# Kernel tuning notes

Measured on AMD Instinct MI355X. Metric: run time of the kernel, lower is better.

## Reference

```python
import jax, jax.numpy as jnp
import numpy as np

B, S, H = 2, 2048, 2048
NUM_HEADS, HEAD_DIM, GROUP_SIZE = 16, 128, 4
NUM_KV_HEADS = NUM_HEADS // GROUP_SIZE
ROPE_THETA = 10000.0


def setup_inputs() -> dict:
    key = jax.random.key(0)
    ks = jax.random.split(key, 10)
    xavier = lambda k, fi, fo: jax.random.uniform(k, (fi, fo), jnp.float32,
                                                  -jnp.sqrt(6.0 / (fi + fo)), jnp.sqrt(6.0 / (fi + fo)))
    hidden_states = jax.random.normal(ks[0], (B, S, H), jnp.float32)
    # causal mask: 1.0 where attention is disallowed (strictly upper triangle)
    mask = jnp.triu(jnp.ones((S, S), jnp.float32), k=1)[None, None, :, :]
    mask = jnp.broadcast_to(mask, (B, 1, S, S))
    return {
        "hidden_states": hidden_states,
        "mask": mask,
        "Wq": xavier(ks[1], H, NUM_HEADS * HEAD_DIM), "bq": jnp.zeros((NUM_HEADS * HEAD_DIM,), jnp.float32),
        "Wk": xavier(ks[2], H, NUM_KV_HEADS * HEAD_DIM), "bk": jnp.zeros((NUM_KV_HEADS * HEAD_DIM,), jnp.float32),
        "Wv": xavier(ks[3], H, NUM_KV_HEADS * HEAD_DIM), "bv": jnp.zeros((NUM_KV_HEADS * HEAD_DIM,), jnp.float32),
        "Wo": xavier(ks[4], NUM_HEADS * HEAD_DIM, H), "bo": jnp.zeros((H,), jnp.float32),
    }


def _apply_rope(q, k):
    # q: [b, s, hq, d], k: [b, s, hk, d]
    s, d = q.shape[1], q.shape[-1]
    inv_freq = 1.0 / (ROPE_THETA ** (jnp.arange(0, d, 2, dtype=jnp.float32) / d))  # [d/2]
    angles = jnp.arange(s, dtype=jnp.float32)[:, None] * inv_freq[None, :]          # [s, d/2]
    cos = jnp.cos(angles)[None, :, None, :]  # [1, s, 1, d/2]
    sin = jnp.sin(angles)[None, :, None, :]

    def rot(x):
        x1, x2 = jnp.split(x, 2, axis=-1)
        return jnp.concatenate([x1 * cos - x2 * sin, x1 * sin + x2 * cos], axis=-1)

    return rot(q), rot(k)


def reference(hidden_states, mask, Wq, bq, Wk, bk, Wv, bv, Wo, bo):
    b, s, _ = hidden_states.shape
    scale = 1.0 / jnp.sqrt(jnp.float32(HEAD_DIM))

    q = (hidden_states @ Wq + bq).reshape(b, s, NUM_HEADS, HEAD_DIM)
    k = (hidden_states @ Wk + bk).reshape(b, s, NUM_KV_HEADS, HEAD_DIM)
    v = (hidden_states @ Wv + bv).reshape(b, s, NUM_KV_HEADS, HEAD_DIM)

    q, k = _apply_rope(q, k)

    q = jnp.transpose(q, (0, 2, 1, 3))  # [b, hq, s, d]
    k = jnp.transpose(k, (0, 2, 1, 3))  # [b, hk, s, d]
    v = jnp.transpose(v, (0, 2, 1, 3))

    new_past_key, new_past_value = k, v

    # GQA: repeat each KV head group_size times
    k_rep = jnp.repeat(k, GROUP_SIZE, axis=1)  # [b, hq, s, d]
    v_rep = jnp.repeat(v, GROUP_SIZE, axis=1)

    attn_scores = jnp.einsum('bhqd,bhkd->bhqk', q, k_rep) * scale  # [b, hq, s, s]
    attn_scores = attn_scores + mask * -1e9
    attn_probs = jax.nn.softmax(attn_scores, axis=-1)
    attn_output = jnp.einsum('bhqk,bhkd->bhqd', attn_probs, v_rep)

    attn_output = attn_output.transpose(0, 2, 1, 3).reshape(b, s, NUM_HEADS * HEAD_DIM)
    attn_output = attn_output @ Wo + bo
    return attn_output, new_past_key, new_past_value
```

## Files before the change

kernel.cpp:

```cpp
#include <hip/hip_runtime.h>
#include <stdint.h>

#define S_LEN 2048
#define HDIM  2048
#define N_HEADS 16
#define HEAD_D 128
#define N_KV 4

typedef unsigned short u16;
typedef __attribute__((ext_vector_type(8))) short bf16x8;
typedef __attribute__((ext_vector_type(4))) float f32x4;

__device__ __forceinline__ u16 f2bf(float f) {
  unsigned u = __float_as_uint(f);
  u += 0x7FFFu + ((u >> 16) & 1u);
  return (u16)(u >> 16);
}

__device__ __forceinline__ void gll16(void* lds, const void* gp) {
  __builtin_amdgcn_global_load_lds(
      (const __attribute__((address_space(1))) void*)gp,
      (__attribute__((address_space(3))) void*)lds, 16, 0, 0);
}

__global__ __launch_bounds__(256) void k_convert(const float* __restrict__ src,
                                                 u16* __restrict__ dst, int n4) {
  int i = blockIdx.x * 256 + threadIdx.x;
  if (i < n4) {
    float4 v = ((const float4*)src)[i];
    ushort4 o;
    o.x = f2bf(v.x); o.y = f2bf(v.y); o.z = f2bf(v.z); o.w = f2bf(v.w);
    ((ushort4*)dst)[i] = o;
  }
}

__global__ __launch_bounds__(256) void k_transpose_w(const float* __restrict__ W,
                                                     u16* __restrict__ Wt,
                                                     int K, int N) {
  __shared__ float tile[64][65];
  int k0 = blockIdx.x * 64, n0 = blockIdx.y * 64;
  int tr = threadIdx.x >> 6, tc = threadIdx.x & 63;
#pragma unroll
  for (int i = 0; i < 16; ++i) {
    int r = tr + i * 4;
    tile[r][tc] = W[(size_t)(k0 + r) * N + n0 + tc];
  }
  __syncthreads();
#pragma unroll
  for (int i = 0; i < 16; ++i) {
    int r = tr + i * 4;
    Wt[(size_t)(n0 + r) * K + k0 + tc] = f2bf(tile[tc][r]);
  }
}

__device__ __forceinline__ void gemm_tile_128(
    const u16* __restrict__ A, const u16* __restrict__ Bt,
    const float* __restrict__ bias, float* __restrict__ C,
    int m0, int n0, int K, int ldc) {
  __shared__ __align__(16) u16 sA[128 * 32];
  __shared__ __align__(16) u16 sB[128 * 32];
  const int tid = threadIdx.x;
  const int lane = tid & 63;
  const int wave = tid >> 6;
  const int quad = lane >> 4;
  const int l15 = lane & 15;
  const int wm = (wave >> 1) << 6;
  const int wn = (wave & 1) << 6;

  f32x4 acc[4][4];
#pragma unroll
  for (int i = 0; i < 4; ++i)
#pragma unroll
    for (int j = 0; j < 4; ++j)
      acc[i][j] = (f32x4){0.f, 0.f, 0.f, 0.f};

  for (int kk = 0; kk < K; kk += 32) {
    __syncthreads();
#pragma unroll
    for (int it = 0; it < 2; ++it) {
      int c = tid + (it << 8);
      int row = c >> 2;
      int ko = (c & 3) << 3;
      gll16((char*)sA + c * 16, A + (size_t)(m0 + row) * K + kk + ko);
      gll16((char*)sB + c * 16, Bt + (size_t)(n0 + row) * K + kk + ko);
    }
    __syncthreads();
    bf16x8 af[4], bfr[4];
#pragma unroll
    for (int i = 0; i < 4; ++i)
      af[i] = *(const bf16x8*)&sA[(wm + (i << 4) + l15) * 32 + quad * 8];
#pragma unroll
    for (int j = 0; j < 4; ++j)
      bfr[j] = *(const bf16x8*)&sB[(wn + (j << 4) + l15) * 32 + quad * 8];
#pragma unroll
    for (int i = 0; i < 4; ++i)
#pragma unroll
      for (int j = 0; j < 4; ++j)
        acc[i][j] = __builtin_amdgcn_mfma_f32_16x16x32_bf16(af[i], bfr[j], acc[i][j], 0, 0, 0);
  }

#pragma unroll
  for (int i = 0; i < 4; ++i) {
    int row = m0 + wm + (i << 4) + quad * 4;
#pragma unroll
    for (int j = 0; j < 4; ++j) {
      int col = n0 + wn + (j << 4) + l15;
      float bv = bias[col];
      float* cp = C + (size_t)row * ldc + col;
#pragma unroll
      for (int r = 0; r < 4; ++r)
        cp[(size_t)r * ldc] = acc[i][j][r] + bv;
    }
  }
}

__global__ __launch_bounds__(256) void k_gemm_qkv(
    const u16* __restrict__ X, const u16* __restrict__ Wqt,
    const u16* __restrict__ Wkt, const u16* __restrict__ Wvt,
    const float* __restrict__ bq, const float* __restrict__ bk,
    const float* __restrict__ bv, float* __restrict__ Qf,
    float* __restrict__ Kf, float* __restrict__ Vf) {
  int m0 = blockIdx.x << 7;
  int by = blockIdx.y;
  const u16* Bt; const float* bias; float* C; int n0, ldc;
  if (by < 16)      { Bt = Wqt; bias = bq; C = Qf; n0 = by << 7;        ldc = 2048; }
  else if (by < 20) { Bt = Wkt; bias = bk; C = Kf; n0 = (by - 16) << 7; ldc = 512;  }
  else              { Bt = Wvt; bias = bv; C = Vf; n0 = (by - 20) << 7; ldc = 512;  }
  gemm_tile_128(X, Bt, bias, C, m0, n0, 2048, ldc);
}

__global__ __launch_bounds__(256) void k_gemm_o(
    const u16* __restrict__ A, const u16* __restrict__ Wot,
    const float* __restrict__ bo, float* __restrict__ C) {
  gemm_tile_128(A, Wot, bo, C, blockIdx.x << 7, blockIdx.y << 7, 2048, 2048);
}

__global__ __launch_bounds__(256) void k_rope(
    const float* __restrict__ Qf, const float* __restrict__ Kf,
    u16* __restrict__ Qbf, u16* __restrict__ Kbf, float* __restrict__ outK) {
  const int bx = blockIdx.x;
  const int b = bx >> 11;
  const int s = bx & 2047;
  const int tid = threadIdx.x;
  const float qscale = 0.08838834764831845f;
  const float c1 = -13.287712379549449f / 64.f;

#pragma unroll
  for (int it = 0; it < 4; ++it) {
    int p = tid + (it << 8);
    int hh = p >> 6;
    int ii = p & 63;
    float ang = (float)s * exp2f((float)ii * c1);
    float cs, sn;
    sincosf(ang, &sn, &cs);
    const float* src = Qf + (size_t)bx * 2048 + hh * 128 + ii;
    float x1 = src[0], x2 = src[64];
    float o1 = (x1 * cs - x2 * sn) * qscale;
    float o2 = (x1 * sn + x2 * cs) * qscale;
    u16* dst = Qbf + ((size_t)(b * N_HEADS + hh) * S_LEN + s) * HEAD_D + ii;
    dst[0] = f2bf(o1);
    dst[64] = f2bf(o2);
  }
  {
    int hh = tid >> 6;
    int ii = tid & 63;
    float ang = (float)s * exp2f((float)ii * c1);
    float cs, sn;
    sincosf(ang, &sn, &cs);
    const float* src = Kf + (size_t)bx * 512 + hh * 128 + ii;
    float x1 = src[0], x2 = src[64];
    float o1 = x1 * cs - x2 * sn;
    float o2 = x1 * sn + x2 * cs;
    size_t idx = ((size_t)(b * N_KV + hh) * S_LEN + s) * HEAD_D + ii;
    Kbf[idx] = f2bf(o1);
    Kbf[idx + 64] = f2bf(o2);
    outK[idx] = o1;
    outK[idx + 64] = o2;
  }
}

__global__ __launch_bounds__(256) void k_vtrans(const float* __restrict__ Vf,
                                                u16* __restrict__ Vt,
                                                float* __restrict__ outV) {
  __shared__ float tile[64][65];
  int s0 = blockIdx.x * 64, d0 = blockIdx.y * 64;
  int z = blockIdx.z;
  int b = z >> 2, kvh = z & 3;
  int tr = threadIdx.x >> 6, tc = threadIdx.x & 63;
#pragma unroll
  for (int i = 0; i < 16; ++i) {
    int r = tr + i * 4;
    float v = Vf[(size_t)(b * S_LEN + s0 + r) * 512 + kvh * 128 + d0 + tc];
    tile[r][tc] = v;
    outV[((size_t)z * S_LEN + s0 + r) * HEAD_D + d0 + tc] = v;
  }
  __syncthreads();
#pragma unroll
  for (int i = 0; i < 16; ++i) {
    int r = tr + i * 4;
    Vt[((size_t)z * HEAD_D + d0 + r) * S_LEN + s0 + tc] = f2bf(tile[tc][r]);
  }
}

__global__ __launch_bounds__(256, 2) void k_attn(
    const u16* __restrict__ Qbf, const u16* __restrict__ Kbf,
    const u16* __restrict__ Vt, u16* __restrict__ attn) {
  __shared__ __align__(16) u16 smem[27136];
  u16* sK = smem;
  u16* sV = smem + 8704;
  u16* sP = smem + 17920;

  const int tid = threadIdx.x;
  const int lane = tid & 63;
  const int wave = tid >> 6;
  const int quad = lane >> 4;
  const int l15 = lane & 15;

  const int qt = blockIdx.x;
  const int b = blockIdx.y >> 4;
  const int h = blockIdx.y & 15;
  const int kvh = h >> 2;
  const int q0 = qt << 7;

  const u16* Qb = Qbf + ((size_t)(b * N_HEADS + h) * S_LEN + q0) * HEAD_D;
  const u16* Kb = Kbf + (size_t)(b * N_KV + kvh) * S_LEN * HEAD_D;
  const u16* Vb = Vt + (size_t)(b * N_KV + kvh) * HEAD_D * S_LEN;

  for (int it = 0; it < 9; ++it) {
    int c = tid + (it << 8);
    if (c < 2176) {
      int row = c / 17;
      int k16 = c - row * 17;
      gll16((char*)smem + c * 16, Qb + (size_t)row * HEAD_D + k16 * 8);
    }
  }
  __syncthreads();

  bf16x8 aq[2][4];
#pragma unroll
  for (int i = 0; i < 2; ++i)
#pragma unroll
    for (int kc = 0; kc < 4; ++kc)
      aq[i][kc] = *(const bf16x8*)&smem[(wave * 32 + i * 16 + l15) * 136 + kc * 32 + quad * 8];

  float mst[2][4], lst[2][4];
  f32x4 oacc[2][8];
#pragma unroll
  for (int i = 0; i < 2; ++i) {
#pragma unroll
    for (int r = 0; r < 4; ++r) { mst[i][r] = -1e30f; lst[i][r] = 0.f; }
#pragma unroll
    for (int n = 0; n < 8; ++n) oacc[i][n] = (f32x4){0.f, 0.f, 0.f, 0.f};
  }

  const int ntiles = 2 * qt + 2;
  for (int t = 0; t < ntiles; ++t) {
    const int kt0 = t << 6;
    __syncthreads();
#pragma unroll
    for (int it = 0; it < 5; ++it) {
      int c = tid + (it << 8);
      if (c < 1088) {
        int row = c / 17;
        int k16 = c - row * 17;
        gll16((char*)sK + c * 16, Kb + (size_t)(kt0 + row) * HEAD_D + k16 * 8);
      }
      if (c < 1152) {
        int d = c / 9;
        int s16 = c - d * 9;
        gll16((char*)sV + c * 16, Vb + (size_t)d * S_LEN + kt0 + s16 * 8);
      }
    }
    __syncthreads();

    f32x4 sc[2][4];
#pragma unroll
    for (int i = 0; i < 2; ++i)
#pragma unroll
      for (int j = 0; j < 4; ++j)
        sc[i][j] = (f32x4){0.f, 0.f, 0.f, 0.f};
#pragma unroll
    for (int kc = 0; kc < 4; ++kc) {
      bf16x8 bk[4];
#pragma unroll
      for (int j = 0; j < 4; ++j)
        bk[j] = *(const bf16x8*)&sK[(j * 16 + l15) * 136 + kc * 32 + quad * 8];
#pragma unroll
      for (int i = 0; i < 2; ++i)
#pragma unroll
        for (int j = 0; j < 4; ++j)
          sc[i][j] = __builtin_amdgcn_mfma_f32_16x16x32_bf16(aq[i][kc], bk[j], sc[i][j], 0, 0, 0);
    }

    if (t >= 2 * qt) {
#pragma unroll
      for (int i = 0; i < 2; ++i) {
        int qrow = q0 + wave * 32 + i * 16 + quad * 4;
#pragma unroll
        for (int j = 0; j < 4; ++j) {
          int col = kt0 + j * 16 + l15;
#pragma unroll
          for (int r = 0; r < 4; ++r)
            if (col > qrow + r) sc[i][j][r] = -1e9f;
        }
      }
    }

#pragma unroll
    for (int i = 0; i < 2; ++i) {
      float al[4];
#pragma unroll
      for (int r = 0; r < 4; ++r) {
        float m = fmaxf(fmaxf(sc[i][0][r], sc[i][1][r]), fmaxf(sc[i][2][r], sc[i][3][r]));
#pragma unroll
        for (int off = 1; off < 16; off <<= 1)
          m = fmaxf(m, __shfl_xor(m, off, 64));
        float mn = fmaxf(mst[i][r], m);
        al[r] = __expf(mst[i][r] - mn);
        mst[i][r] = mn;
      }
      float rs[4] = {0.f, 0.f, 0.f, 0.f};
#pragma unroll
      for (int j = 0; j < 4; ++j)
#pragma unroll
        for (int r = 0; r < 4; ++r) {
          float p = __expf(sc[i][j][r] - mst[i][r]);
          rs[r] += p;
          sP[(wave * 32 + i * 16 + quad * 4 + r) * 72 + j * 16 + l15] = f2bf(p);
        }
#pragma unroll
      for (int r = 0; r < 4; ++r) {
        float s = rs[r];
#pragma unroll
        for (int off = 1; off < 16; off <<= 1)
          s += __shfl_xor(s, off, 64);
        lst[i][r] = lst[i][r] * al[r] + s;
#pragma unroll
        for (int n = 0; n < 8; ++n)
          oacc[i][n][r] *= al[r];
      }
    }
    __syncthreads();

#pragma unroll
    for (int kc = 0; kc < 2; ++kc) {
      bf16x8 ap[2];
#pragma unroll
      for (int i = 0; i < 2; ++i)
        ap[i] = *(const bf16x8*)&sP[(wave * 32 + i * 16 + l15) * 72 + kc * 32 + quad * 8];
#pragma unroll
      for (int n = 0; n < 8; ++n) {
        bf16x8 bv = *(const bf16x8*)&sV[(n * 16 + l15) * 72 + kc * 32 + quad * 8];
#pragma unroll
        for (int i = 0; i < 2; ++i)
          oacc[i][n] = __builtin_amdgcn_mfma_f32_16x16x32_bf16(ap[i], bv, oacc[i][n], 0, 0, 0);
      }
    }
  }

#pragma unroll
  for (int i = 0; i < 2; ++i)
#pragma unroll
    for (int r = 0; r < 4; ++r) {
      int row = q0 + wave * 32 + i * 16 + quad * 4 + r;
      float inv = 1.0f / lst[i][r];
      u16* op = attn + ((size_t)b * S_LEN + row) * HDIM + h * HEAD_D;
#pragma unroll
      for (int n = 0; n < 8; ++n)
        op[n * 16 + l15] = f2bf(oacc[i][n][r] * inv);
    }
}

extern "C" void kernel_launch(void* const* d_in, const int* in_sizes, int n_in,
                              void* d_out, int out_size, void* d_ws, size_t ws_size,
                              hipStream_t stream) {
  (void)in_sizes; (void)n_in; (void)out_size; (void)ws_size;
  const float* hs = (const float*)d_in[0];
  const float* Wq = (const float*)d_in[2];
  const float* bq = (const float*)d_in[3];
  const float* Wk = (const float*)d_in[4];
  const float* bk = (const float*)d_in[5];
  const float* Wv = (const float*)d_in[6];
  const float* bv = (const float*)d_in[7];
  const float* Wo = (const float*)d_in[8];
  const float* bo = (const float*)d_in[9];
  float* out = (float*)d_out;

  char* ws = (char*)d_ws;
  u16* Xbf   = (u16*)(ws + 0);
  u16* Wqt   = (u16*)(ws + 16777216);
  u16* Wkt   = (u16*)(ws + 25165824);
  u16* Wvt   = (u16*)(ws + 27262976);
  u16* Wot   = (u16*)(ws + 29360128);
  float* Qf  = (float*)(ws + 37748736);
  float* Kf  = (float*)(ws + 71303168);
  float* Vf  = (float*)(ws + 79691776);
  u16* Qbf   = (u16*)(ws + 88080384);
  u16* Kbf   = (u16*)(ws + 104857600);
  u16* Vtb   = (u16*)(ws + 109051904);
  u16* attnb = (u16*)(ws + 37748736);

  k_convert<<<8192, 256, 0, stream>>>(hs, Xbf, 2097152);
  k_transpose_w<<<dim3(32, 32), 256, 0, stream>>>(Wq, Wqt, 2048, 2048);
  k_transpose_w<<<dim3(32, 8), 256, 0, stream>>>(Wk, Wkt, 2048, 512);
  k_transpose_w<<<dim3(32, 8), 256, 0, stream>>>(Wv, Wvt, 2048, 512);
  k_transpose_w<<<dim3(32, 32), 256, 0, stream>>>(Wo, Wot, 2048, 2048);
  k_gemm_qkv<<<dim3(32, 24), 256, 0, stream>>>(Xbf, Wqt, Wkt, Wvt, bq, bk, bv, Qf, Kf, Vf);
  k_rope<<<4096, 256, 0, stream>>>(Qf, Kf, Qbf, Kbf, out + 8388608);
  k_vtrans<<<dim3(32, 2, 8), 256, 0, stream>>>(Vf, Vtb, out + 10485760);
  k_attn<<<dim3(16, 32), 256, 0, stream>>>(Qbf, Kbf, Vtb, attnb);
  k_gemm_o<<<dim3(32, 16), 256, 0, stream>>>(attnb, Wot, bo, out);
}
```

Before: 411.8 us.

## Shrink attention query tile to 64 rows and schedule heaviest causal tiles first

The attention kernel now has each block handle 64 query rows (16 per wave) instead of 128, doubling the grid to 1024 blocks. It loads Q straight from global into registers and drops the Q staging in LDS. Block order is reversed so the longest causal rows launch first, and the K/V tile loads are spread across separate threads. Smaller LDS and register use allow three blocks per CU, which should improve load balance and occupancy. The trade-off is that each K/V tile loaded into LDS is reused by half as many query rows, and the barrier between the P writes and the PV reads was removed.

```diff
diff --git a/kernel.cpp b/kernel.cpp
--- a/kernel.cpp
+++ b/kernel.cpp
@@ -202,10 +202,10 @@
   }
 }
 
-__global__ __launch_bounds__(256, 2) void k_attn(
+__global__ __launch_bounds__(256, 3) void k_attn(
     const u16* __restrict__ Qbf, const u16* __restrict__ Kbf,
     const u16* __restrict__ Vt, u16* __restrict__ attn) {
-  __shared__ __align__(16) u16 smem[27136];
+  __shared__ __align__(16) u16 smem[22528];
   u16* sK = smem;
   u16* sV = smem + 8704;
   u16* sP = smem + 17920;
@@ -216,159 +216,124 @@
   const int quad = lane >> 4;
   const int l15 = lane & 15;
 
-  const int qt = blockIdx.x;
-  const int b = blockIdx.y >> 4;
-  const int h = blockIdx.y & 15;
+  const int qt = 31 - blockIdx.y;
+  const int bh = blockIdx.x;
+  const int b = bh >> 4;
+  const int h = bh & 15;
   const int kvh = h >> 2;
-  const int q0 = qt << 7;
+  const int q0 = qt << 6;
 
   const u16* Qb = Qbf + ((size_t)(b * N_HEADS + h) * S_LEN + q0) * HEAD_D;
   const u16* Kb = Kbf + (size_t)(b * N_KV + kvh) * S_LEN * HEAD_D;
   const u16* Vb = Vt + (size_t)(b * N_KV + kvh) * HEAD_D * S_LEN;
 
-  for (int it = 0; it < 9; ++it) {
-    int c = tid + (it << 8);
-    if (c < 2176) {
-      int row = c / 17;
-      int k16 = c - row * 17;
-      gll16((char*)smem + c * 16, Qb + (size_t)row * HEAD_D + k16 * 8);
-    }
-  }
-  __syncthreads();
-
-  bf16x8 aq[2][4];
-#pragma unroll
-  for (int i = 0; i < 2; ++i)
-#pragma unroll
-    for (int kc = 0; kc < 4; ++kc)
-      aq[i][kc] = *(const bf16x8*)&smem[(wave * 32 + i * 16 + l15) * 136 + kc * 32 + quad * 8];
-
-  float mst[2][4], lst[2][4];
-  f32x4 oacc[2][8];
-#pragma unroll
-  for (int i = 0; i < 2; ++i) {
-#pragma unroll
-    for (int r = 0; r < 4; ++r) { mst[i][r] = -1e30f; lst[i][r] = 0.f; }
-#pragma unroll
-    for (int n = 0; n < 8; ++n) oacc[i][n] = (f32x4){0.f, 0.f, 0.f, 0.f};
-  }
-
-  const int ntiles = 2 * qt + 2;
+  bf16x8 aq[4];
+#pragma unroll
+  for (int kc = 0; kc < 4; ++kc)
+    aq[kc] = *(const bf16x8*)(Qb + (size_t)(wave * 16 + l15) * HEAD_D + kc * 32 + quad * 8);
+
+  float mst[4], lst[4];
+  f32x4 oacc[8];
+#pragma unroll
+  for (int r = 0; r < 4; ++r) { mst[r] = -1e30f; lst[r] = 0.f; }
+#pragma unroll
+  for (int n = 0; n < 8; ++n) oacc[n] = (f32x4){0.f, 0.f, 0.f, 0.f};
+
+  const int ntiles = qt + 1;
   for (int t = 0; t < ntiles; ++t) {
     const int kt0 = t << 6;
     __syncthreads();
 #pragma unroll
-    for (int it = 0; it < 5; ++it) {
+    for (int it = 0; it < 9; ++it) {
       int c = tid + (it << 8);
       if (c < 1088) {
         int row = c / 17;
         int k16 = c - row * 17;
         gll16((char*)sK + c * 16, Kb + (size_t)(kt0 + row) * HEAD_D + k16 * 8);
-      }
-      if (c < 1152) {
-        int d = c / 9;
-        int s16 = c - d * 9;
-        gll16((char*)sV + c * 16, Vb + (size_t)d * S_LEN + kt0 + s16 * 8);
+      } else if (c < 2240) {
+        int vv = c - 1088;
+        int d = vv / 9;
+        int s16 = vv - d * 9;
+        gll16((char*)sV + vv * 16, Vb + (size_t)d * S_LEN + kt0 + s16 * 8);
       }
     }
     __syncthreads();
 
-    f32x4 sc[2][4];
-#pragma unroll
-    for (int i = 0; i < 2; ++i)
-#pragma unroll
-      for (int j = 0; j < 4; ++j)
-        sc[i][j] = (f32x4){0.f, 0.f, 0.f, 0.f};
+    f32x4 sc[4];
+#pragma unroll
+    for (int j = 0; j < 4; ++j) sc[j] = (f32x4){0.f, 0.f, 0.f, 0.f};
 #pragma unroll
     for (int kc = 0; kc < 4; ++kc) {
-      bf16x8 bk[4];
-#pragma unroll
-      for (int j = 0; j < 4; ++j)
-        bk[j] = *(const bf16x8*)&sK[(j * 16 + l15) * 136 + kc * 32 + quad * 8];
-#pragma unroll
-      for (int i = 0; i < 2; ++i)
-#pragma unroll
-        for (int j = 0; j < 4; ++j)
-          sc[i][j] = __builtin_amdgcn_mfma_f32_16x16x32_bf16(aq[i][kc], bk[j], sc[i][j], 0, 0, 0);
-    }
-
-    if (t >= 2 * qt) {
-#pragma unroll
-      for (int i = 0; i < 2; ++i) {
-        int qrow = q0 + wave * 32 + i * 16 + quad * 4;
-#pragma unroll
-        for (int j = 0; j < 4; ++j) {
-          int col = kt0 + j * 16 + l15;
-#pragma unroll
-          for (int r = 0; r < 4; ++r)
-            if (col > qrow + r) sc[i][j][r] = -1e9f;
-        }
-      }
-    }
-
-#pragma unroll
-    for (int i = 0; i < 2; ++i) {
-      float al[4];
+#pragma unroll
+      for (int j = 0; j < 4; ++j) {
+        bf16x8 bk = *(const bf16x8*)&sK[(j * 16 + l15) * 136 + kc * 32 + quad * 8];
+        sc[j] = __builtin_amdgcn_mfma_f32_16x16x32_bf16(aq[kc], bk, sc[j], 0, 0, 0);
+      }
+    }
+
+    if (t == qt) {
+      int qrow = q0 + wave * 16 + quad * 4;
+#pragma unroll
+      for (int j = 0; j < 4; ++j) {
+        int col = kt0 + j * 16 + l15;
+#pragma unroll
+        for (int r = 0; r < 4; ++r)
+          if (col > qrow + r) sc[j][r] = -1e9f;
+      }
+    }
+
+    float al[4];
+#pragma unroll
+    for (int r = 0; r < 4; ++r) {
+      float m = fmaxf(fmaxf(sc[0][r], sc[1][r]), fmaxf(sc[2][r], sc[3][r]));
+#pragma unroll
+      for (int off = 1; off < 16; off <<= 1)
+        m = fmaxf(m, __shfl_xor(m, off, 64));
+      float mn = fmaxf(mst[r], m);
+      al[r] = __expf(mst[r] - mn);
+      mst[r] = mn;
+    }
+    float rs[4] = {0.f, 0.f, 0.f, 0.f};
+#pragma unroll
+    for (int j = 0; j < 4; ++j)
 #pragma unroll
       for (int r = 0; r < 4; ++r) {
-        float m = fmaxf(fmaxf(sc[i][0][r], sc[i][1][r]), fmaxf(sc[i][2][r], sc[i][3][r]));
-#pragma unroll
-        for (int off = 1; off < 16; off <<= 1)
-          m = fmaxf(m, __shfl_xor(m, off, 64));
-        float mn = fmaxf(mst[i][r], m);
-        al[r] = __expf(mst[i][r] - mn);
-        mst[i][r] = mn;
-      }
-      float rs[4] = {0.f, 0.f, 0.f, 0.f};
-#pragma unroll
-      for (int j = 0; j < 4; ++j)
-#pragma unroll
-        for (int r = 0; r < 4; ++r) {
-          float p = __expf(sc[i][j][r] - mst[i][r]);
-          rs[r] += p;
-          sP[(wave * 32 + i * 16 + quad * 4 + r) * 72 + j * 16 + l15] = f2bf(p);
-        }
-#pragma unroll
-      for (int r = 0; r < 4; ++r) {
-        float s = rs[r];
-#pragma unroll
-        for (int off = 1; off < 16; off <<= 1)
-          s += __shfl_xor(s, off, 64);
-        lst[i][r] = lst[i][r] * al[r] + s;
-#pragma unroll
-        for (int n = 0; n < 8; ++n)
-          oacc[i][n][r] *= al[r];
-      }
-    }
-    __syncthreads();
+        float p = __expf(sc[j][r] - mst[r]);
+        rs[r] += p;
+        sP[(wave * 16 + quad * 4 + r) * 72 + j * 16 + l15] = f2bf(p);
+      }
+#pragma unroll
+    for (int r = 0; r < 4; ++r) {
+      float s = rs[r];
+#pragma unroll
+      for (int off = 1; off < 16; off <<= 1)
+        s += __shfl_xor(s, off, 64);
+      lst[r] = lst[r] * al[r] + s;
+#pragma unroll
+      for (int n = 0; n < 8; ++n)
+        oacc[n][r] *= al[r];
+    }
 
 #pragma unroll
     for (int kc = 0; kc < 2; ++kc) {
-      bf16x8 ap[2];
-#pragma unroll
-      for (int i = 0; i < 2; ++i)
-        ap[i] = *(const bf16x8*)&sP[(wave * 32 + i * 16 + l15) * 72 + kc * 32 + quad * 8];
+      bf16x8 ap = *(const bf16x8*)&sP[(wave * 16 + l15) * 72 + kc * 32 + quad * 8];
 #pragma unroll
       for (int n = 0; n < 8; ++n) {
         bf16x8 bv = *(const bf16x8*)&sV[(n * 16 + l15) * 72 + kc * 32 + quad * 8];
-#pragma unroll
-        for (int i = 0; i < 2; ++i)
-          oacc[i][n] = __builtin_amdgcn_mfma_f32_16x16x32_bf16(ap[i], bv, oacc[i][n], 0, 0, 0);
-      }
-    }
-  }
-
-#pragma unroll
-  for (int i = 0; i < 2; ++i)
-#pragma unroll
-    for (int r = 0; r < 4; ++r) {
-      int row = q0 + wave * 32 + i * 16 + quad * 4 + r;
-      float inv = 1.0f / lst[i][r];
-      u16* op = attn + ((size_t)b * S_LEN + row) * HDIM + h * HEAD_D;
-#pragma unroll
-      for (int n = 0; n < 8; ++n)
-        op[n * 16 + l15] = f2bf(oacc[i][n][r] * inv);
-    }
+        oacc[n] = __builtin_amdgcn_mfma_f32_16x16x32_bf16(ap, bv, oacc[n], 0, 0, 0);
+      }
+    }
+  }
+
+#pragma unroll
+  for (int r = 0; r < 4; ++r) {
+    int row = q0 + wave * 16 + quad * 4 + r;
+    float inv = 1.0f / lst[r];
+    u16* op = attn + ((size_t)b * S_LEN + row) * HDIM + h * HEAD_D;
+#pragma unroll
+    for (int n = 0; n < 8; ++n)
+      op[n * 16 + l15] = f2bf(oacc[n][r] * inv);
+  }
 }
 
 extern "C" void kernel_launch(void* const* d_in, const int* in_sizes, int n_in,
@@ -408,6 +373,6 @@
   k_gemm_qkv<<<dim3(32, 24), 256, 0, stream>>>(Xbf, Wqt, Wkt, Wvt, bq, bk, bv, Qf, Kf, Vf);
   k_rope<<<4096, 256, 0, stream>>>(Qf, Kf, Qbf, Kbf, out + 8388608);
   k_vtrans<<<dim3(32, 2, 8), 256, 0, stream>>>(Vf, Vtb, out + 10485760);
-  k_attn<<<dim3(16, 32), 256, 0, stream>>>(Qbf, Kbf, Vtb, attnb);
+  k_attn<<<dim3(32, 32), 256, 0, stream>>>(Qbf, Kbf, Vtb, attnb);
   k_gemm_o<<<dim3(32, 16), 256, 0, stream>>>(attnb, Wot, bo, out);
 }
```

After: 381.4 us. -7.4%, faster.
